# Performance work log

Measured on AMD Instinct MI355X. Metric: run time of the kernel, lower is better.

The kernel has to match this reference:

```python
import jax, jax.numpy as jnp
import numpy as np

N_NODES = 100000
EPS = 1e-12


def _sage_conv(x, src, dst, Wl, bl, Wr):
    # PyG SAGEConv (aggr='mean'): lin_l(mean of neighbor msgs) + lin_r(x)
    msgs = x[src]                                                # [E, d] gather
    agg = jax.ops.segment_sum(msgs, dst, num_segments=N_NODES)  # [N, d] scatter-add
    deg = jax.ops.segment_sum(jnp.ones((src.shape[0],), x.dtype), dst,
                              num_segments=N_NODES)             # [N]
    agg = agg / jnp.maximum(deg, 1.0)[:, None]                  # scatter-mean
    return agg @ Wl + bl + x @ Wr


def setup_inputs() -> dict:
    key = jax.random.key(0)
    ks = jax.random.split(key, 16)
    d_in, d_h = 64, 64
    E = 1600000
    s = 0.1
    inp = {
        'x': jax.random.normal(ks[0], (N_NODES, d_in), jnp.float32),
        'edge_index': jax.random.randint(ks[1], (2, E), 0, N_NODES, jnp.int64),
    }
    dims = [(d_in, d_h), (d_h, d_h), (d_h, d_h), (d_h, d_h)]
    for i, (di, do) in enumerate(dims, start=1):
        inp[f'Wl{i}'] = s * jax.random.normal(ks[3 * i - 1], (di, do), jnp.float32)
        inp[f'bl{i}'] = jnp.zeros((do,), jnp.float32)
        inp[f'Wr{i}'] = s * jax.random.normal(ks[3 * i], (di, do), jnp.float32)
    return inp


def reference(x, edge_index, Wl1, bl1, Wr1, Wl2, bl2, Wr2, Wl3, bl3, Wr3, Wl4, bl4, Wr4):
    src, dst = edge_index[0], edge_index[1]
    # dropout is identity in eval mode
    h1 = jax.nn.relu(_sage_conv(x, src, dst, Wl1, bl1, Wr1))
    h2 = jax.nn.relu(_sage_conv(h1, src, dst, Wl2, bl2, Wr2)) + h1
    h3 = jax.nn.relu(_sage_conv(h2, src, dst, Wl3, bl3, Wr3)) + h2
    out = _sage_conv(h3, src, dst, Wl4, bl4, Wr4)
    # F.normalize(p=2, dim=1, eps=1e-12)
    norm = jnp.maximum(jnp.linalg.norm(out, axis=1, keepdims=True), EPS)
    return out / norm
```

## Files before the change

### kernel.cpp

```cpp
#include <hip/hip_runtime.h>


#include <hip/hip_bf16.h>

static inline size_t al256(size_t x) { return (x + 255) & ~(size_t)255; }

#define EPB 8192

typedef _Float16 f16x8 __attribute__((ext_vector_type(8)));
typedef float f32x4 __attribute__((ext_vector_type(4)));

__global__ void k_detect(const unsigned int* __restrict__ raw, int E, int* __restrict__ flag) {
  int nz = 0;
#pragma unroll
  for (int k = 0; k < 64; ++k) {
    int i = threadIdx.x + (k << 8);
    if (i < E && raw[2 * (size_t)i + 1] != 0u) nz = 1;
  }
  unsigned long long b = __ballot(nz != 0);
  if ((threadIdx.x & 63) == 0 && b) atomicOr(flag, 1);
}

__global__ __launch_bounds__(256) void k_bcount(const unsigned int* __restrict__ raw, int E,
                                                int span, const int* __restrict__ flag,
                                                int* __restrict__ bucketCount) {
  __shared__ int lh[256];
  int t = threadIdx.x;
  lh[t] = 0;
  __syncthreads();
  int f = *flag;
  int base = blockIdx.x * EPB;
#pragma unroll 4
  for (int k = 0; k < EPB / 256; ++k) {
    int i = base + k * 256 + t;
    if (i < E) {
      int dst = f ? (int)raw[E + i] : (int)raw[2 * (size_t)(E + i)];
      atomicAdd(&lh[dst / span], 1);
    }
  }
  __syncthreads();
  int c = lh[t];
  if (c) atomicAdd(&bucketCount[t], c);
}

__global__ void k_bscan(const int* __restrict__ bucketCount, int* __restrict__ boff,
                        int* __restrict__ cursorB, int* __restrict__ rs, int N, int E) {
  __shared__ int sa[256], sb[256];
  int t = threadIdx.x;
  int v = bucketCount[t];
  sa[t] = v;
  __syncthreads();
  int* s = sa;
  int* d = sb;
  for (int off = 1; off < 256; off <<= 1) {
    d[t] = s[t] + (t >= off ? s[t - off] : 0);
    __syncthreads();
    int* tmp = s; s = d; d = tmp;
  }
  int inc = s[t];
  int ex = inc - v;
  boff[t] = ex;
  cursorB[t] = ex;
  if (t == 255) boff[256] = inc;
  if (t == 0) rs[N] = E;
}

__global__ __launch_bounds__(256) void k_bscatter(const unsigned int* __restrict__ raw, int E,
                                                  int span, const int* __restrict__ flag,
                                                  int* __restrict__ cursorB,
                                                  uint2* __restrict__ bdata) {
  __shared__ int lh[256], lcur[256], gbase[256];
  int t = threadIdx.x;
  lh[t] = 0;
  lcur[t] = 0;
  __syncthreads();
  int f = *flag;
  int base = blockIdx.x * EPB;
#pragma unroll 4
  for (int k = 0; k < EPB / 256; ++k) {
    int i = base + k * 256 + t;
    if (i < E) {
      int dst = f ? (int)raw[E + i] : (int)raw[2 * (size_t)(E + i)];
      atomicAdd(&lh[dst / span], 1);
    }
  }
  __syncthreads();
  int c = lh[t];
  gbase[t] = c ? atomicAdd(&cursorB[t], c) : 0;
  __syncthreads();
#pragma unroll 4
  for (int k = 0; k < EPB / 256; ++k) {
    int i = base + k * 256 + t;
    if (i < E) {
      int s_, d_;
      if (f) { s_ = (int)raw[i]; d_ = (int)raw[E + i]; }
      else   { s_ = (int)raw[2 * (size_t)i]; d_ = (int)raw[2 * (size_t)(E + i)]; }
      int b = d_ / span;
      int pos = atomicAdd(&lcur[b], 1);
      bdata[(size_t)gbase[b] + pos] = make_uint2((unsigned)s_, (unsigned)d_);
    }
  }
}

__global__ __launch_bounds__(256) void k_bbuild(const uint2* __restrict__ bdata,
                                                const int* __restrict__ boff, int span, int N,
                                                int* __restrict__ csr, int* __restrict__ rs,
                                                float* __restrict__ invdeg) {
  __shared__ int cnt[512], sa[512], sb[512], cur[512];
  int b = blockIdx.x;
  int t = threadIdx.x;
  int node0 = b * span;
  int beg = boff[b], end = boff[b + 1];
  cnt[t] = 0;
  cnt[t + 256] = 0;
  __syncthreads();
  for (int i = beg + t; i < end; i += 256) {
    int d = (int)bdata[i].y - node0;
    atomicAdd(&cnt[d], 1);
  }
  __syncthreads();
  sa[t] = cnt[t];
  sa[t + 256] = cnt[t + 256];
  __syncthreads();
  int* s = sa;
  int* d = sb;
  for (int off = 1; off < 512; off <<= 1) {
    d[t] = s[t] + (t >= off ? s[t - off] : 0);
    int i2 = t + 256;
    d[i2] = s[i2] + (i2 >= off ? s[i2 - off] : 0);
    __syncthreads();
    int* tmp = s; s = d; d = tmp;
  }
  int ex0 = s[t] - cnt[t];
  int ex1 = s[t + 256] - cnt[t + 256];
  cur[t] = ex0;
  cur[t + 256] = ex1;
  if (t < span) {
    int node = node0 + t;
    if (node < N) {
      rs[node] = beg + ex0;
      invdeg[node] = 1.0f / fmaxf((float)cnt[t], 1.0f);
    }
  }
  int t2 = t + 256;
  if (t2 < span) {
    int node = node0 + t2;
    if (node < N) {
      rs[node] = beg + ex1;
      invdeg[node] = 1.0f / fmaxf((float)cnt[t2], 1.0f);
    }
  }
  __syncthreads();
  for (int i = beg + t; i < end; i += 256) {
    uint2 p = bdata[i];
    int dd = (int)p.y - node0;
    int pos = atomicAdd(&cur[dd], 1);
    csr[beg + pos] = (int)p.x;
  }
}

__global__ __launch_bounds__(256) void k_gemm(
    const float* __restrict__ h, const float* __restrict__ Wl,
    const float* __restrict__ Wr, const float* __restrict__ bl,
    unsigned short* __restrict__ Pf, float* __restrict__ R, int n) {
  __shared__ uint4 hAu[512];
  char* hAraw = (char*)hAu;
  int t = threadIdx.x;
  int n0 = blockIdx.x * 64;
  int w = t >> 6;
  int l = t & 63;
  int lo16 = l & 15;
  int g = l >> 4;

#pragma unroll
  for (int c = 0; c < 4; ++c) {
    int idx = t + c * 256;
    int row = idx >> 4;
    int fc = idx & 15;
    int nn = n0 + row;
    float4 hv = (nn < n) ? *(const float4*)&h[(size_t)nn * 64 + fc * 4]
                         : make_float4(0.f, 0.f, 0.f, 0.f);
    union { _Float16 p[4]; uint2 u; } cv;
    cv.p[0] = (_Float16)hv.x; cv.p[1] = (_Float16)hv.y;
    cv.p[2] = (_Float16)hv.z; cv.p[3] = (_Float16)hv.w;
    int byte = (row * 128 + fc * 8) ^ ((row & 7) << 4);
    *(uint2*)(hAraw + byte) = cv.u;
  }

  const float* Wsel = (w < 2) ? Wl : Wr;
  int colbase = (w & 1) * 32;
  f16x8 bfr[2][2];
#pragma unroll
  for (int nf = 0; nf < 2; ++nf) {
    int j = colbase + nf * 16 + lo16;
#pragma unroll
    for (int kk = 0; kk < 2; ++kk) {
      int k0 = kk * 32 + g * 8;
      f16x8 bb;
#pragma unroll
      for (int s = 0; s < 8; ++s) bb[s] = (_Float16)Wsel[(k0 + s) * 64 + j];
      bfr[nf][kk] = bb;
    }
  }
  __syncthreads();

  f32x4 acc[4][2];
#pragma unroll
  for (int mf = 0; mf < 4; ++mf)
#pragma unroll
    for (int nf = 0; nf < 2; ++nf) acc[mf][nf] = (f32x4){0.f, 0.f, 0.f, 0.f};

#pragma unroll
  for (int mf = 0; mf < 4; ++mf) {
    int row = mf * 16 + lo16;
    int swz = (row & 7) << 4;
    f16x8 av0 = *(const f16x8*)(hAraw + row * 128 + ((g * 16) ^ swz));
    f16x8 av1 = *(const f16x8*)(hAraw + row * 128 + ((64 + g * 16) ^ swz));
#pragma unroll
    for (int nf = 0; nf < 2; ++nf) {
      acc[mf][nf] = __builtin_amdgcn_mfma_f32_16x16x32_f16(av0, bfr[nf][0], acc[mf][nf], 0, 0, 0);
      acc[mf][nf] = __builtin_amdgcn_mfma_f32_16x16x32_f16(av1, bfr[nf][1], acc[mf][nf], 0, 0, 0);
    }
  }

#pragma unroll
  for (int nf = 0; nf < 2; ++nf) {
    int col = colbase + nf * 16 + lo16;
    float bv = (w >= 2) ? bl[col] : 0.f;
#pragma unroll
    for (int mf = 0; mf < 4; ++mf) {
#pragma unroll
      for (int r = 0; r < 4; ++r) {
        int grow = n0 + mf * 16 + g * 4 + r;
        if (grow < n) {
          float v = acc[mf][nf][r];
          if (w < 2) {
            union { _Float16 hh; unsigned short us; } cv;
            cv.hh = (_Float16)v;
            Pf[(size_t)grow * 64 + col] = cv.us;
          } else {
            R[(size_t)grow * 64 + col] = v + bv;
          }
        }
      }
    }
  }
}

template <int MODE>
__global__ __launch_bounds__(256) void k_gather(
    const uint2* __restrict__ P2, const float* __restrict__ R,
    const float* __restrict__ hres, const int* __restrict__ csr,
    const int* __restrict__ rs, const float* __restrict__ invdeg,
    float* __restrict__ hout, int n) {
  typedef _Float16 h2 __attribute__((ext_vector_type(2)));
  union HU { unsigned u32; h2 h; };
  int l = threadIdx.x & 63;
  int v = (blockIdx.x << 2) + (threadIdx.x >> 6);
  if (v >= n) return;
  int q = l & 15;
  int g = l >> 4;
  int beg = rs[v], end = rs[v + 1];
  float idg = invdeg[v];
  float4 rv = *(const float4*)&R[((size_t)v << 6) + (q << 2)];
  float4 hv = make_float4(0.f, 0.f, 0.f, 0.f);
  if (MODE == 1) hv = *(const float4*)&hres[((size_t)v << 6) + (q << 2)];

  float s0 = 0.f, s1 = 0.f, s2 = 0.f, s3 = 0.f;
  int i = beg;
  int rem = end - beg;
  int myidx = 0;
  if (rem > 0) myidx = csr[i + (q < rem ? q : (rem - 1))];
  for (; i + 16 <= end;) {
    int inext = i + 16;
    int remn = end - inext;
    int nxt = 0;
    if (remn > 0) nxt = csr[inext + (q < remn ? q : (remn - 1))];
    h2 a0 = (h2)0, a1 = (h2)0;
#pragma unroll
    for (int t = 0; t < 4; ++t) {
      int sel = __shfl(myidx, 4 * t + g, 64);
      uint2 u = P2[(unsigned)((sel << 4) + q)];
      HU b0, b1;
      b0.u32 = u.x;
      b1.u32 = u.y;
      a0 += b0.h;
      a1 += b1.h;
    }
    s0 += (float)a0[0];
    s1 += (float)a0[1];
    s2 += (float)a1[0];
    s3 += (float)a1[1];
    myidx = nxt;
    i = inext;
  }
  int r = end - i;
  if (r > 0) {
    h2 a0 = (h2)0, a1 = (h2)0;
#pragma unroll
    for (int t = 0; t < 4; ++t) {
      if (4 * t >= r) break;
      int e = 4 * t + g;
      int sel = __shfl(myidx, e < r ? e : 0, 64);
      if (e < r) {
        uint2 u = P2[(unsigned)((sel << 4) + q)];
        HU b0, b1;
        b0.u32 = u.x;
        b1.u32 = u.y;
        a0 += b0.h;
        a1 += b1.h;
      }
    }
    s0 += (float)a0[0];
    s1 += (float)a0[1];
    s2 += (float)a1[0];
    s3 += (float)a1[1];
  }
  s0 += __shfl_xor(s0, 16, 64); s0 += __shfl_xor(s0, 32, 64);
  s1 += __shfl_xor(s1, 16, 64); s1 += __shfl_xor(s1, 32, 64);
  s2 += __shfl_xor(s2, 16, 64); s2 += __shfl_xor(s2, 32, 64);
  s3 += __shfl_xor(s3, 16, 64); s3 += __shfl_xor(s3, 32, 64);

  if (l < 16) {
    float4 o;
    o.x = s0 * idg + rv.x;
    o.y = s1 * idg + rv.y;
    o.z = s2 * idg + rv.z;
    o.w = s3 * idg + rv.w;
    if (MODE == 0) {
      o.x = fmaxf(o.x, 0.f); o.y = fmaxf(o.y, 0.f);
      o.z = fmaxf(o.z, 0.f); o.w = fmaxf(o.w, 0.f);
    } else if (MODE == 1) {
      o.x = fmaxf(o.x, 0.f) + hv.x; o.y = fmaxf(o.y, 0.f) + hv.y;
      o.z = fmaxf(o.z, 0.f) + hv.z; o.w = fmaxf(o.w, 0.f) + hv.w;
    } else {
      float sq = o.x * o.x + o.y * o.y + o.z * o.z + o.w * o.w;
#pragma unroll
      for (int m = 1; m < 16; m <<= 1) sq += __shfl_xor(sq, m, 64);
      float nrm = fmaxf(sqrtf(sq), 1e-12f);
      o.x /= nrm; o.y /= nrm; o.z /= nrm; o.w /= nrm;
    }
    *(float4*)&hout[((size_t)v << 6) + (q << 2)] = o;
  }
}

extern "C" void kernel_launch(void* const* d_in, const int* in_sizes, int n_in,
                              void* d_out, int out_size, void* d_ws, size_t ws_size,
                              hipStream_t stream) {
  const float* x = (const float*)d_in[0];
  const unsigned int* eraw = (const unsigned int*)d_in[1];
  const float* Wl[4] = {(const float*)d_in[2], (const float*)d_in[5],
                        (const float*)d_in[8], (const float*)d_in[11]};
  const float* blv[4] = {(const float*)d_in[3], (const float*)d_in[6],
                         (const float*)d_in[9], (const float*)d_in[12]};
  const float* Wr[4] = {(const float*)d_in[4], (const float*)d_in[7],
                        (const float*)d_in[10], (const float*)d_in[13]};
  const int N = in_sizes[0] / 64;
  const int E = in_sizes[1] / 2;
  const int span = (N + 255) / 256;
  float* out = (float*)d_out;

  char* w = (char*)d_ws;
  size_t off = 0;
  int* flag = (int*)(w + off);        off = al256(off + 4);
  int* bucketCount = (int*)(w + off); off = al256(off + 256 * 4);
  int* boff = (int*)(w + off);        off = al256(off + 257 * 4);
  int* cursorB = (int*)(w + off);     off = al256(off + 256 * 4);
  int* csr = (int*)(w + off);         off = al256(off + (size_t)E * 4);
  float* invdeg = (float*)(w + off);  off = al256(off + (size_t)N * 4);
  int* rs = (int*)(w + off);          off = al256(off + (size_t)(N + 1) * 4);
  uint2* bdata = (uint2*)(w + off);   off = al256(off + (size_t)E * 8);
  float* hA = (float*)(w + off);      off = al256(off + (size_t)N * 64 * 4);
  unsigned short* Pf = (unsigned short*)(w + off); off = al256(off + (size_t)N * 64 * 2);
  float* R = (float*)(w + off);       off = al256(off + (size_t)N * 64 * 4);

  hipMemsetAsync(flag, 0, 4, stream);
  hipMemsetAsync(bucketCount, 0, 256 * 4, stream);

  int eb = (E + EPB - 1) / EPB;
  k_detect<<<1, 256, 0, stream>>>(eraw, E, flag);
  k_bcount<<<eb, 256, 0, stream>>>(eraw, E, span, flag, bucketCount);
  k_bscan<<<1, 256, 0, stream>>>(bucketCount, boff, cursorB, rs, N, E);
  k_bscatter<<<eb, 256, 0, stream>>>(eraw, E, span, flag, cursorB, bdata);
  k_bbuild<<<256, 256, 0, stream>>>(bdata, boff, span, N, csr, rs, invdeg);

  int gb = (N + 63) / 64;
  int nb4 = (N + 3) / 4;
  const uint2* P2 = (const uint2*)Pf;
  k_gemm<<<gb, 256, 0, stream>>>(x, Wl[0], Wr[0], blv[0], Pf, R, N);
  k_gather<0><<<nb4, 256, 0, stream>>>(P2, R, nullptr, csr, rs, invdeg, hA, N);
  k_gemm<<<gb, 256, 0, stream>>>(hA, Wl[1], Wr[1], blv[1], Pf, R, N);
  k_gather<1><<<nb4, 256, 0, stream>>>(P2, R, hA, csr, rs, invdeg, out, N);
  k_gemm<<<gb, 256, 0, stream>>>(out, Wl[2], Wr[2], blv[2], Pf, R, N);
  k_gather<1><<<nb4, 256, 0, stream>>>(P2, R, out, csr, rs, invdeg, hA, N);
  k_gemm<<<gb, 256, 0, stream>>>(hA, Wl[3], Wr[3], blv[3], Pf, R, N);
  k_gather<2><<<nb4, 256, 0, stream>>>(P2, R, nullptr, csr, rs, invdeg, out, N);
}
```

Measured before the change: 328.4 us.

## Store intermediate activations and root term in fp16, pack bucket edges into 32 bits

Hidden activations and the root-projection term R are now stored as fp16 instead of fp32, so the GEMM and gather kernels read and write half the bytes for these tensors. The GEMM gets a template variant that loads fp16 input directly without converting. Bucketed edge data is packed into one 32-bit word (local dst in the high bits, src in the low 17 bits), which halves the scatter and build traffic. The costs are lower precision on residual and hidden values, and a packing scheme that assumes node ids fit in 17 bits and a bucket span of at most 512 nodes.

New measurement: 318.1 us. 3.1% less time.

```diff
diff --git a/kernel.cpp b/kernel.cpp
--- a/kernel.cpp
+++ b/kernel.cpp
@@ -68,7 +68,7 @@
 __global__ __launch_bounds__(256) void k_bscatter(const unsigned int* __restrict__ raw, int E,
                                                   int span, const int* __restrict__ flag,
                                                   int* __restrict__ cursorB,
-                                                  uint2* __restrict__ bdata) {
+                                                  unsigned* __restrict__ bdata) {
   __shared__ int lh[256], lcur[256], gbase[256];
   int t = threadIdx.x;
   lh[t] = 0;
@@ -97,12 +97,12 @@
       else   { s_ = (int)raw[2 * (size_t)i]; d_ = (int)raw[2 * (size_t)(E + i)]; }
       int b = d_ / span;
       int pos = atomicAdd(&lcur[b], 1);
-      bdata[(size_t)gbase[b] + pos] = make_uint2((unsigned)s_, (unsigned)d_);
-    }
-  }
-}
-
-__global__ __launch_bounds__(256) void k_bbuild(const uint2* __restrict__ bdata,
+      bdata[(size_t)gbase[b] + pos] = ((unsigned)(d_ - b * span) << 17) | (unsigned)s_;
+    }
+  }
+}
+
+__global__ __launch_bounds__(256) void k_bbuild(const unsigned* __restrict__ bdata,
                                                 const int* __restrict__ boff, int span, int N,
                                                 int* __restrict__ csr, int* __restrict__ rs,
                                                 float* __restrict__ invdeg) {
@@ -115,8 +115,7 @@
   cnt[t + 256] = 0;
   __syncthreads();
   for (int i = beg + t; i < end; i += 256) {
-    int d = (int)bdata[i].y - node0;
-    atomicAdd(&cnt[d], 1);
+    atomicAdd(&cnt[bdata[i] >> 17], 1);
   }
   __syncthreads();
   sa[t] = cnt[t];
@@ -152,17 +151,17 @@
   }
   __syncthreads();
   for (int i = beg + t; i < end; i += 256) {
-    uint2 p = bdata[i];
-    int dd = (int)p.y - node0;
-    int pos = atomicAdd(&cur[dd], 1);
-    csr[beg + pos] = (int)p.x;
-  }
-}
-
+    unsigned p = bdata[i];
+    int pos = atomicAdd(&cur[p >> 17], 1);
+    csr[beg + pos] = (int)(p & 0x1FFFFu);
+  }
+}
+
+template <int IT>
 __global__ __launch_bounds__(256) void k_gemm(
-    const float* __restrict__ h, const float* __restrict__ Wl,
+    const void* __restrict__ hv_, const float* __restrict__ Wl,
     const float* __restrict__ Wr, const float* __restrict__ bl,
-    unsigned short* __restrict__ Pf, float* __restrict__ R, int n) {
+    unsigned short* __restrict__ Pf, unsigned short* __restrict__ R16, int n) {
   __shared__ uint4 hAu[512];
   char* hAraw = (char*)hAu;
   int t = threadIdx.x;
@@ -178,13 +177,21 @@
     int row = idx >> 4;
     int fc = idx & 15;
     int nn = n0 + row;
-    float4 hv = (nn < n) ? *(const float4*)&h[(size_t)nn * 64 + fc * 4]
-                         : make_float4(0.f, 0.f, 0.f, 0.f);
-    union { _Float16 p[4]; uint2 u; } cv;
-    cv.p[0] = (_Float16)hv.x; cv.p[1] = (_Float16)hv.y;
-    cv.p[2] = (_Float16)hv.z; cv.p[3] = (_Float16)hv.w;
+    uint2 u = make_uint2(0u, 0u);
+    if (nn < n) {
+      if (IT == 0) {
+        const float* h = (const float*)hv_;
+        float4 hv = *(const float4*)&h[(size_t)nn * 64 + fc * 4];
+        union { _Float16 p[4]; uint2 u; } cv;
+        cv.p[0] = (_Float16)hv.x; cv.p[1] = (_Float16)hv.y;
+        cv.p[2] = (_Float16)hv.z; cv.p[3] = (_Float16)hv.w;
+        u = cv.u;
+      } else {
+        u = *(const uint2*)((const char*)hv_ + (size_t)nn * 128 + fc * 8);
+      }
+    }
     int byte = (row * 128 + fc * 8) ^ ((row & 7) << 4);
-    *(uint2*)(hAraw + byte) = cv.u;
+    *(uint2*)(hAraw + byte) = u;
   }
 
   const float* Wsel = (w < 2) ? Wl : Wr;
@@ -234,12 +241,13 @@
         int grow = n0 + mf * 16 + g * 4 + r;
         if (grow < n) {
           float v = acc[mf][nf][r];
+          union { _Float16 hh; unsigned short us; } cv;
           if (w < 2) {
-            union { _Float16 hh; unsigned short us; } cv;
             cv.hh = (_Float16)v;
             Pf[(size_t)grow * 64 + col] = cv.us;
           } else {
-            R[(size_t)grow * 64 + col] = v + bv;
+            cv.hh = (_Float16)(v + bv);
+            R16[(size_t)grow * 64 + col] = cv.us;
           }
         }
       }
@@ -249,12 +257,13 @@
 
 template <int MODE>
 __global__ __launch_bounds__(256) void k_gather(
-    const uint2* __restrict__ P2, const float* __restrict__ R,
-    const float* __restrict__ hres, const int* __restrict__ csr,
+    const uint2* __restrict__ P2, const unsigned short* __restrict__ R16,
+    const unsigned short* __restrict__ hres, const int* __restrict__ csr,
     const int* __restrict__ rs, const float* __restrict__ invdeg,
-    float* __restrict__ hout, int n) {
+    void* __restrict__ hout, int n) {
   typedef _Float16 h2 __attribute__((ext_vector_type(2)));
   union HU { unsigned u32; h2 h; };
+  union Q4 { uint2 u; _Float16 hh[4]; };
   int l = threadIdx.x & 63;
   int v = (blockIdx.x << 2) + (threadIdx.x >> 6);
   if (v >= n) return;
@@ -262,9 +271,11 @@
   int g = l >> 4;
   int beg = rs[v], end = rs[v + 1];
   float idg = invdeg[v];
-  float4 rv = *(const float4*)&R[((size_t)v << 6) + (q << 2)];
-  float4 hv = make_float4(0.f, 0.f, 0.f, 0.f);
-  if (MODE == 1) hv = *(const float4*)&hres[((size_t)v << 6) + (q << 2)];
+  Q4 rq;
+  rq.u = *(const uint2*)((const char*)R16 + (size_t)v * 128 + q * 8);
+  Q4 hq;
+  hq.u = make_uint2(0u, 0u);
+  if (MODE == 1) hq.u = *(const uint2*)((const char*)hres + (size_t)v * 128 + q * 8);
 
   float s0 = 0.f, s1 = 0.f, s2 = 0.f, s3 = 0.f;
   int i = beg;
@@ -323,16 +334,18 @@
 
   if (l < 16) {
     float4 o;
-    o.x = s0 * idg + rv.x;
-    o.y = s1 * idg + rv.y;
-    o.z = s2 * idg + rv.z;
-    o.w = s3 * idg + rv.w;
+    o.x = s0 * idg + (float)rq.hh[0];
+    o.y = s1 * idg + (float)rq.hh[1];
+    o.z = s2 * idg + (float)rq.hh[2];
+    o.w = s3 * idg + (float)rq.hh[3];
     if (MODE == 0) {
       o.x = fmaxf(o.x, 0.f); o.y = fmaxf(o.y, 0.f);
       o.z = fmaxf(o.z, 0.f); o.w = fmaxf(o.w, 0.f);
     } else if (MODE == 1) {
-      o.x = fmaxf(o.x, 0.f) + hv.x; o.y = fmaxf(o.y, 0.f) + hv.y;
-      o.z = fmaxf(o.z, 0.f) + hv.z; o.w = fmaxf(o.w, 0.f) + hv.w;
+      o.x = fmaxf(o.x, 0.f) + (float)hq.hh[0];
+      o.y = fmaxf(o.y, 0.f) + (float)hq.hh[1];
+      o.z = fmaxf(o.z, 0.f) + (float)hq.hh[2];
+      o.w = fmaxf(o.w, 0.f) + (float)hq.hh[3];
     } else {
       float sq = o.x * o.x + o.y * o.y + o.z * o.z + o.w * o.w;
 #pragma unroll
@@ -340,7 +353,14 @@
       float nrm = fmaxf(sqrtf(sq), 1e-12f);
       o.x /= nrm; o.y /= nrm; o.z /= nrm; o.w /= nrm;
     }
-    *(float4*)&hout[((size_t)v << 6) + (q << 2)] = o;
+    if (MODE == 2) {
+      *(float4*)&((float*)hout)[((size_t)v << 6) + (q << 2)] = o;
+    } else {
+      Q4 oq;
+      oq.hh[0] = (_Float16)o.x; oq.hh[1] = (_Float16)o.y;
+      oq.hh[2] = (_Float16)o.z; oq.hh[3] = (_Float16)o.w;
+      *(uint2*)((char*)hout + (size_t)v * 128 + q * 8) = oq.u;
+    }
   }
 }
 
@@ -369,10 +389,11 @@
   int* csr = (int*)(w + off);         off = al256(off + (size_t)E * 4);
   float* invdeg = (float*)(w + off);  off = al256(off + (size_t)N * 4);
   int* rs = (int*)(w + off);          off = al256(off + (size_t)(N + 1) * 4);
-  uint2* bdata = (uint2*)(w + off);   off = al256(off + (size_t)E * 8);
-  float* hA = (float*)(w + off);      off = al256(off + (size_t)N * 64 * 4);
+  unsigned* bdata = (unsigned*)(w + off); off = al256(off + (size_t)E * 4);
+  unsigned short* hA = (unsigned short*)(w + off); off = al256(off + (size_t)N * 64 * 2);
+  unsigned short* hB = (unsigned short*)(w + off); off = al256(off + (size_t)N * 64 * 2);
   unsigned short* Pf = (unsigned short*)(w + off); off = al256(off + (size_t)N * 64 * 2);
-  float* R = (float*)(w + off);       off = al256(off + (size_t)N * 64 * 4);
+  unsigned short* R16 = (unsigned short*)(w + off); off = al256(off + (size_t)N * 64 * 2);
 
   hipMemsetAsync(flag, 0, 4, stream);
   hipMemsetAsync(bucketCount, 0, 256 * 4, stream);
@@ -387,12 +408,12 @@
   int gb = (N + 63) / 64;
   int nb4 = (N + 3) / 4;
   const uint2* P2 = (const uint2*)Pf;
-  k_gemm<<<gb, 256, 0, stream>>>(x, Wl[0], Wr[0], blv[0], Pf, R, N);
-  k_gather<0><<<nb4, 256, 0, stream>>>(P2, R, nullptr, csr, rs, invdeg, hA, N);
-  k_gemm<<<gb, 256, 0, stream>>>(hA, Wl[1], Wr[1], blv[1], Pf, R, N);
-  k_gather<1><<<nb4, 256, 0, stream>>>(P2, R, hA, csr, rs, invdeg, out, N);
-  k_gemm<<<gb, 256, 0, stream>>>(out, Wl[2], Wr[2], blv[2], Pf, R, N);
-  k_gather<1><<<nb4, 256, 0, stream>>>(P2, R, out, csr, rs, invdeg, hA, N);
-  k_gemm<<<gb, 256, 0, stream>>>(hA, Wl[3], Wr[3], blv[3], Pf, R, N);
-  k_gather<2><<<nb4, 256, 0, stream>>>(P2, R, nullptr, csr, rs, invdeg, out, N);
-}
+  k_gemm<0><<<gb, 256, 0, stream>>>(x, Wl[0], Wr[0], blv[0], Pf, R16, N);
+  k_gather<0><<<nb4, 256, 0, stream>>>(P2, R16, nullptr, csr, rs, invdeg, hA, N);
+  k_gemm<1><<<gb, 256, 0, stream>>>(hA, Wl[1], Wr[1], blv[1], Pf, R16, N);
+  k_gather<1><<<nb4, 256, 0, stream>>>(P2, R16, hA, csr, rs, invdeg, hB, N);
+  k_gemm<1><<<gb, 256, 0, stream>>>(hB, Wl[2], Wr[2], blv[2], Pf, R16, N);
+  k_gather<1><<<nb4, 256, 0, stream>>>(P2, R16, hB, csr, rs, invdeg, hA, N);
+  k_gemm<1><<<gb, 256, 0, stream>>>(hA, Wl[3], Wr[3], blv[3], Pf, R16, N);
+  k_gather<2><<<nb4, 256, 0, stream>>>(P2, R16, nullptr, csr, rs, invdeg, out, N);
+}
```
